# Performance work log

Hardware: AMD Instinct MI355X
Metric: run time of the kernel (lower is better)

## Reference

```python
import jax, jax.numpy as jnp
import numpy as np

N_NODES = 50000
N_EDGES = 800000
HIDDEN = 128
MLP_DIM = 64

def setup_inputs() -> dict:
    key = jax.random.key(0)
    k1, k2, k3, k4 = jax.random.split(key, 4)
    node_emb = jax.random.normal(k1, (N_NODES, HIDDEN), dtype=jnp.float32)
    edge_index = jax.random.randint(k2, (2, N_EDGES), 0, N_NODES, dtype=jnp.int64)
    # Xavier-uniform init like the torch module
    lim1 = float(np.sqrt(6.0 / (2 * HIDDEN + MLP_DIM)))
    lim2 = float(np.sqrt(6.0 / (MLP_DIM + 1)))
    W1 = jax.random.uniform(k3, (2 * HIDDEN, MLP_DIM), minval=-lim1, maxval=lim1, dtype=jnp.float32)
    b1 = jnp.zeros((MLP_DIM,), dtype=jnp.float32)
    W2 = jax.random.uniform(k4, (MLP_DIM, 1), minval=-lim2, maxval=lim2, dtype=jnp.float32)
    b2 = jnp.zeros((1,), dtype=jnp.float32)
    return {"node_emb": node_emb, "edge_index": edge_index, "W1": W1, "b1": b1, "W2": W2, "b2": b2}

def reference(node_emb, edge_index, W1, b1, W2, b2):
    src, dst = edge_index[0], edge_index[1]
    emb_src = node_emb[src]                      # [E, H] gather
    emb_dst = node_emb[dst]                      # [E, H] gather
    edge_emb = jnp.concatenate([emb_src, emb_dst], axis=1)  # [E, 2H]
    h = jax.nn.relu(edge_emb @ W1 + b1)          # [E, MLP_DIM]
    edge_logits = h @ W2 + b2                    # [E, 1]
    return edge_logits
```

## Files before the change

kernel.cpp:

```cpp
#include <hip/hip_runtime.h>
#include <hip/hip_bf16.h>


#define HIDDEN 128

typedef __attribute__((ext_vector_type(8))) short bf16x8;
typedef __attribute__((ext_vector_type(4))) float f32x4;
typedef __attribute__((ext_vector_type(8))) _Float16 half8;
typedef __attribute__((ext_vector_type(4))) _Float16 half4f;

__device__ inline unsigned short f32_to_bf16(float f) {
    unsigned int u = __float_as_uint(f);
    unsigned int r = (u + 0x7fffu + ((u >> 16) & 1u)) >> 16;
    return (unsigned short)r;
}

__global__ __launch_bounds__(256, 4) void precompute_pq_mfma(
    const float* __restrict__ node_emb,
    const float* __restrict__ W1,
    const float* __restrict__ b1,
    _Float16* __restrict__ PQ,
    int n_nodes)
{
    __shared__ unsigned short Bt[128 * 136];

    const int t = threadIdx.x;
    const int wave = t >> 6, lane = t & 63;
    const int l15 = lane & 15;
    const int kq = (lane >> 4) * 8;
    const int m0 = blockIdx.x * 64;
    const int node = m0 + wave * 16 + l15;
    const bool valid = (node < n_nodes);

    const float* arow = node_emb + (size_t)(valid ? node : 0) * HIDDEN + kq;
    float4 aLo[4], aHi[4];
    #pragma unroll
    for (int i = 0; i < 4; ++i) {
        if (valid) {
            aLo[i] = *(const float4*)(arow + i * 32);
            aHi[i] = *(const float4*)(arow + i * 32 + 4);
        } else {
            aLo[i] = make_float4(0.f, 0.f, 0.f, 0.f);
            aHi[i] = aLo[i];
        }
    }

    #pragma unroll
    for (int it = 0; it < 16; ++it) {
        int slot = it * 256 + t;
        int r = slot >> 4;
        int c4 = (slot & 15) * 4;
        float4 v = *(const float4*)&W1[r * 64 + c4];
        int j = (r < 128) ? c4 : (c4 + 64);
        int k = r & 127;
        Bt[(j + 0) * 136 + k] = f32_to_bf16(v.x);
        Bt[(j + 1) * 136 + k] = f32_to_bf16(v.y);
        Bt[(j + 2) * 136 + k] = f32_to_bf16(v.z);
        Bt[(j + 3) * 136 + k] = f32_to_bf16(v.w);
    }
    __syncthreads();

    f32x4 acc[8];
    #pragma unroll
    for (int c = 0; c < 8; ++c) acc[c] = (f32x4){0.f, 0.f, 0.f, 0.f};

    #pragma unroll
    for (int k0i = 0; k0i < 4; ++k0i) {
        union { bf16x8 v; __hip_bfloat162 h[4]; } ua;
        ua.h[0] = __float22bfloat162_rn(make_float2(aLo[k0i].x, aLo[k0i].y));
        ua.h[1] = __float22bfloat162_rn(make_float2(aLo[k0i].z, aLo[k0i].w));
        ua.h[2] = __float22bfloat162_rn(make_float2(aHi[k0i].x, aHi[k0i].y));
        ua.h[3] = __float22bfloat162_rn(make_float2(aHi[k0i].z, aHi[k0i].w));
        const int kbase = k0i * 32 + kq;
        #pragma unroll
        for (int c = 0; c < 8; ++c) {
            bf16x8 wf = *(const bf16x8*)&Bt[(c * 16 + l15) * 136 + kbase];
            acc[c] = __builtin_amdgcn_mfma_f32_16x16x32_bf16(wf, ua.v, acc[c], 0, 0, 0);
        }
    }

    if (valid) {
        const int rbase = (lane >> 4) * 4;
        float4 bias[4];
        #pragma unroll
        for (int c = 0; c < 4; ++c) bias[c] = *(const float4*)&b1[c * 16 + rbase];
        _Float16* drow = PQ + (size_t)node * HIDDEN;
        #pragma unroll
        for (int c = 0; c < 8; ++c) {
            half4f v;
            if (c < 4) {
                const float* bf = (const float*)&bias[c];
                #pragma unroll
                for (int reg = 0; reg < 4; ++reg)
                    v[reg] = (_Float16)(acc[c][reg] + bf[reg]);
            } else {
                #pragma unroll
                for (int reg = 0; reg < 4; ++reg)
                    v[reg] = (_Float16)acc[c][reg];
            }
            *(half4f*)&drow[c * 16 + rbase] = v;
        }
    }
}

__global__ __launch_bounds__(256) void edge_mlp16(
    const _Float16* __restrict__ PQ,
    const int* __restrict__ edge_index,
    const float* __restrict__ W2,
    const float* __restrict__ b2,
    float* __restrict__ out,
    int E)
{
    const int t = threadIdx.x;
    const int g = t & 7;
    const int slot = t >> 3;
    const int e0 = blockIdx.x * 64 + slot;
    const int e1 = e0 + 32;

    float4 wA = *(const float4*)&W2[g * 8];
    float4 wB = *(const float4*)&W2[g * 8 + 4];

    const int src0 = __builtin_nontemporal_load(&edge_index[e0]);
    const int dst0 = __builtin_nontemporal_load(&edge_index[E + e0]);
    const int src1 = __builtin_nontemporal_load(&edge_index[e1]);
    const int dst1 = __builtin_nontemporal_load(&edge_index[E + e1]);

    half8 p0 = *(const half8*)&PQ[(size_t)src0 * HIDDEN + g * 8];
    half8 q0 = *(const half8*)&PQ[(size_t)dst0 * HIDDEN + 64 + g * 8];
    half8 p1 = *(const half8*)&PQ[(size_t)src1 * HIDDEN + g * 8];
    half8 q1 = *(const half8*)&PQ[(size_t)dst1 * HIDDEN + 64 + g * 8];

    const float* wa = (const float*)&wA;
    const float* wb = (const float*)&wB;
    float s0 = 0.f, s1 = 0.f;
    #pragma unroll
    for (int i = 0; i < 4; ++i) {
        s0 = fmaf(fmaxf((float)p0[i] + (float)q0[i], 0.f), wa[i], s0);
        s1 = fmaf(fmaxf((float)p1[i] + (float)q1[i], 0.f), wa[i], s1);
    }
    #pragma unroll
    for (int i = 0; i < 4; ++i) {
        s0 = fmaf(fmaxf((float)p0[i + 4] + (float)q0[i + 4], 0.f), wb[i], s0);
        s1 = fmaf(fmaxf((float)p1[i + 4] + (float)q1[i + 4], 0.f), wb[i], s1);
    }

    s0 += __shfl_xor(s0, 1, 64);  s1 += __shfl_xor(s1, 1, 64);
    s0 += __shfl_xor(s0, 2, 64);  s1 += __shfl_xor(s1, 2, 64);
    s0 += __shfl_xor(s0, 4, 64);  s1 += __shfl_xor(s1, 4, 64);

    if (g == 0) {
        float bb = b2[0];
        __builtin_nontemporal_store(s0 + bb, &out[e0]);
        __builtin_nontemporal_store(s1 + bb, &out[e1]);
    }
}

extern "C" void kernel_launch(void* const* d_in, const int* in_sizes, int n_in,
                              void* d_out, int out_size, void* d_ws, size_t ws_size,
                              hipStream_t stream) {
    const float* node_emb   = (const float*)d_in[0];
    const int*   edge_index = (const int*)d_in[1];
    const float* W1 = (const float*)d_in[2];
    const float* b1 = (const float*)d_in[3];
    const float* W2 = (const float*)d_in[4];
    const float* b2 = (const float*)d_in[5];
    float* out = (float*)d_out;

    const int n_nodes = in_sizes[0] / HIDDEN;
    const int E = in_sizes[1] / 2;

    _Float16* PQ = (_Float16*)d_ws;

    const int grid1 = (n_nodes + 63) / 64;
    precompute_pq_mfma<<<grid1, 256, 0, stream>>>(node_emb, W1, b1, PQ, n_nodes);

    const int grid2 = E / 64;
    edge_mlp16<<<grid2, 256, 0, stream>>>(PQ, edge_index, W2, b2, out, E);
}
```

Baseline: 113.7 us.

## Pre-transpose W1 to bf16 once and DMA it into LDS; batch four edges per thread

Adds a small kernel that converts W1 to a padded, transposed bf16 layout in workspace. Each precompute block then copies that layout straight into LDS with global_load_lds, replacing the per-block fp32 load, conversion and scattered LDS stores. The edge kernel now handles four edges per thread group instead of two, halving the grid and putting more independent gathers in flight. The cost is one extra kernel launch and higher register use in the edge kernel.

```diff
diff --git a/kernel.cpp b/kernel.cpp
--- a/kernel.cpp
+++ b/kernel.cpp
@@ -5,9 +5,13 @@
 #define HIDDEN 128
 
 typedef __attribute__((ext_vector_type(8))) short bf16x8;
+typedef __attribute__((ext_vector_type(8))) unsigned short ushort8;
 typedef __attribute__((ext_vector_type(4))) float f32x4;
 typedef __attribute__((ext_vector_type(8))) _Float16 half8;
 typedef __attribute__((ext_vector_type(4))) _Float16 half4f;
+
+#define AS_GLOBAL __attribute__((address_space(1)))
+#define AS_LDS    __attribute__((address_space(3)))
 
 __device__ inline unsigned short f32_to_bf16(float f) {
     unsigned int u = __float_as_uint(f);
@@ -15,9 +19,25 @@
     return (unsigned short)r;
 }
 
+__global__ __launch_bounds__(256) void build_wt(
+    const float* __restrict__ W1,
+    unsigned short* __restrict__ Wt)
+{
+    const int gid = blockIdx.x * 256 + threadIdx.x;
+    const int j  = gid >> 4;
+    const int k0 = (gid & 15) * 8;
+    const int rbase = k0 + ((j >= 64) ? 128 : 0);
+    const int col = j & 63;
+    ushort8 o;
+    #pragma unroll
+    for (int i = 0; i < 8; ++i)
+        o[i] = f32_to_bf16(W1[(rbase + i) * 64 + col]);
+    *(ushort8*)&Wt[j * 136 + k0] = o;
+}
+
 __global__ __launch_bounds__(256, 4) void precompute_pq_mfma(
     const float* __restrict__ node_emb,
-    const float* __restrict__ W1,
+    const unsigned short* __restrict__ Wt,
     const float* __restrict__ b1,
     _Float16* __restrict__ PQ,
     int n_nodes)
@@ -32,6 +52,24 @@
     const int node = m0 + wave * 16 + l15;
     const bool valid = (node < n_nodes);
 
+    {
+        const char* gsrc = (const char*)Wt;
+        char* ldst = (char*)Bt;
+        #pragma unroll
+        for (int it = 0; it < 8; ++it) {
+            const int off = it * 4096 + wave * 1024;
+            __builtin_amdgcn_global_load_lds(
+                (const AS_GLOBAL void*)(gsrc + off + lane * 16),
+                (AS_LDS void*)(ldst + off), 16, 0, 0);
+        }
+        if (wave < 2) {
+            const int off = 32768 + wave * 1024;
+            __builtin_amdgcn_global_load_lds(
+                (const AS_GLOBAL void*)(gsrc + off + lane * 16),
+                (AS_LDS void*)(ldst + off), 16, 0, 0);
+        }
+    }
+
     const float* arow = node_emb + (size_t)(valid ? node : 0) * HIDDEN + kq;
     float4 aLo[4], aHi[4];
     #pragma unroll
@@ -43,20 +81,6 @@
             aLo[i] = make_float4(0.f, 0.f, 0.f, 0.f);
             aHi[i] = aLo[i];
         }
-    }
-
-    #pragma unroll
-    for (int it = 0; it < 16; ++it) {
-        int slot = it * 256 + t;
-        int r = slot >> 4;
-        int c4 = (slot & 15) * 4;
-        float4 v = *(const float4*)&W1[r * 64 + c4];
-        int j = (r < 128) ? c4 : (c4 + 64);
-        int k = r & 127;
-        Bt[(j + 0) * 136 + k] = f32_to_bf16(v.x);
-        Bt[(j + 1) * 136 + k] = f32_to_bf16(v.y);
-        Bt[(j + 2) * 136 + k] = f32_to_bf16(v.z);
-        Bt[(j + 3) * 136 + k] = f32_to_bf16(v.w);
     }
     __syncthreads();
 
@@ -114,44 +138,50 @@
     const int t = threadIdx.x;
     const int g = t & 7;
     const int slot = t >> 3;
-    const int e0 = blockIdx.x * 64 + slot;
-    const int e1 = e0 + 32;
+    const int ebase = blockIdx.x * 128 + slot;
 
     float4 wA = *(const float4*)&W2[g * 8];
     float4 wB = *(const float4*)&W2[g * 8 + 4];
-
-    const int src0 = __builtin_nontemporal_load(&edge_index[e0]);
-    const int dst0 = __builtin_nontemporal_load(&edge_index[E + e0]);
-    const int src1 = __builtin_nontemporal_load(&edge_index[e1]);
-    const int dst1 = __builtin_nontemporal_load(&edge_index[E + e1]);
-
-    half8 p0 = *(const half8*)&PQ[(size_t)src0 * HIDDEN + g * 8];
-    half8 q0 = *(const half8*)&PQ[(size_t)dst0 * HIDDEN + 64 + g * 8];
-    half8 p1 = *(const half8*)&PQ[(size_t)src1 * HIDDEN + g * 8];
-    half8 q1 = *(const half8*)&PQ[(size_t)dst1 * HIDDEN + 64 + g * 8];
-
     const float* wa = (const float*)&wA;
     const float* wb = (const float*)&wB;
-    float s0 = 0.f, s1 = 0.f;
-    #pragma unroll
-    for (int i = 0; i < 4; ++i) {
-        s0 = fmaf(fmaxf((float)p0[i] + (float)q0[i], 0.f), wa[i], s0);
-        s1 = fmaf(fmaxf((float)p1[i] + (float)q1[i], 0.f), wa[i], s1);
-    }
-    #pragma unroll
-    for (int i = 0; i < 4; ++i) {
-        s0 = fmaf(fmaxf((float)p0[i + 4] + (float)q0[i + 4], 0.f), wb[i], s0);
-        s1 = fmaf(fmaxf((float)p1[i + 4] + (float)q1[i + 4], 0.f), wb[i], s1);
-    }
-
-    s0 += __shfl_xor(s0, 1, 64);  s1 += __shfl_xor(s1, 1, 64);
-    s0 += __shfl_xor(s0, 2, 64);  s1 += __shfl_xor(s1, 2, 64);
-    s0 += __shfl_xor(s0, 4, 64);  s1 += __shfl_xor(s1, 4, 64);
+
+    int src[4], dst[4];
+    #pragma unroll
+    for (int j = 0; j < 4; ++j) {
+        src[j] = __builtin_nontemporal_load(&edge_index[ebase + 32 * j]);
+        dst[j] = __builtin_nontemporal_load(&edge_index[E + ebase + 32 * j]);
+    }
+
+    half8 p[4], q[4];
+    #pragma unroll
+    for (int j = 0; j < 4; ++j) {
+        p[j] = *(const half8*)&PQ[(size_t)src[j] * HIDDEN + g * 8];
+        q[j] = *(const half8*)&PQ[(size_t)dst[j] * HIDDEN + 64 + g * 8];
+    }
+
+    float s[4] = {0.f, 0.f, 0.f, 0.f};
+    #pragma unroll
+    for (int j = 0; j < 4; ++j) {
+        #pragma unroll
+        for (int i = 0; i < 4; ++i)
+            s[j] = fmaf(fmaxf((float)p[j][i] + (float)q[j][i], 0.f), wa[i], s[j]);
+        #pragma unroll
+        for (int i = 0; i < 4; ++i)
+            s[j] = fmaf(fmaxf((float)p[j][i + 4] + (float)q[j][i + 4], 0.f), wb[i], s[j]);
+    }
+
+    #pragma unroll
+    for (int j = 0; j < 4; ++j) {
+        s[j] += __shfl_xor(s[j], 1, 64);
+        s[j] += __shfl_xor(s[j], 2, 64);
+        s[j] += __shfl_xor(s[j], 4, 64);
+    }
 
     if (g == 0) {
-        float bb = b2[0];
-        __builtin_nontemporal_store(s0 + bb, &out[e0]);
-        __builtin_nontemporal_store(s1 + bb, &out[e1]);
+        const float bb = b2[0];
+        #pragma unroll
+        for (int j = 0; j < 4; ++j)
+            __builtin_nontemporal_store(s[j] + bb, &out[ebase + 32 * j]);
     }
 }
 
@@ -170,10 +200,14 @@
     const int E = in_sizes[1] / 2;
 
     _Float16* PQ = (_Float16*)d_ws;
+    unsigned short* Wt = (unsigned short*)((char*)d_ws +
+                         (size_t)n_nodes * HIDDEN * sizeof(_Float16));
+
+    build_wt<<<8, 256, 0, stream>>>(W1, Wt);
 
     const int grid1 = (n_nodes + 63) / 64;
-    precompute_pq_mfma<<<grid1, 256, 0, stream>>>(node_emb, W1, b1, PQ, n_nodes);
-
-    const int grid2 = E / 64;
+    precompute_pq_mfma<<<grid1, 256, 0, stream>>>(node_emb, Wt, b1, PQ, n_nodes);
+
+    const int grid2 = E / 128;
     edge_mlp16<<<grid2, 256, 0, stream>>>(PQ, edge_index, W2, b2, out, E);
 }
```

New measurement: 112.7 us. About the same (-0.9%).
